# Performance work log

Hardware: AMD Instinct MI355X
Metric: run time of the kernel (lower is better)

Reference implementation:

```python
import jax, jax.numpy as jnp
import numpy as np


def _conv(x, w, pad):
    return jax.lax.conv_general_dilated(
        x, w, (1, 1), [(pad, pad), (pad, pad)],
        dimension_numbers=('NCHW', 'OIHW', 'NCHW'))


def _avgpool2(x):
    B, C, H, W = x.shape
    return x.reshape(B, C, H // 2, 2, W // 2, 2).mean(axis=(3, 5))


def setup_inputs() -> dict:
    key = jax.random.key(0)
    ks = jax.random.split(key, 10)
    B = 1024
    x = jax.random.uniform(ks[0], (B, 1, 28, 28), jnp.float32)
    # depthwise-separable conv params (in=1 -> depthwise is a plain 3x3 conv)
    dw_w = jax.random.normal(ks[1], (1, 1, 3, 3), jnp.float32) * 0.3
    pw_w = jax.random.normal(ks[2], (32, 1, 1, 1), jnp.float32) * 0.3
    pw_b = jax.random.normal(ks[3], (32,), jnp.float32) * 0.05
    # fixed 4-qubit entangling unitary (real orthogonal 16x16), stand-in for tq.RandomLayer(n_ops=8)
    U = jnp.asarray(np.linalg.qr(np.random.default_rng(0).standard_normal((16, 16)))[0],
                    jnp.float32)
    fus_w = jax.random.normal(ks[4], (128, 36, 3, 3), jnp.float32) * (1.0 / np.sqrt(36 * 9))
    fus_b = jax.random.normal(ks[5], (128,), jnp.float32) * 0.05
    F = 128 * 7 * 7
    cls_w = jax.random.normal(ks[6], (10, F), jnp.float32) * (1.0 / np.sqrt(F))
    cls_b = jax.random.normal(ks[7], (10,), jnp.float32) * 0.05
    reg_w = jax.random.normal(ks[8], (1, F), jnp.float32) * (1.0 / np.sqrt(F))
    reg_b = jax.random.normal(ks[9], (1,), jnp.float32) * 0.05
    return {'x': x, 'dw_w': dw_w, 'pw_w': pw_w, 'pw_b': pw_b, 'U': U,
            'fus_w': fus_w, 'fus_b': fus_b, 'cls_w': cls_w, 'cls_b': cls_b,
            'reg_w': reg_w, 'reg_b': reg_b}


def _quantum_patches(x, U):
    # x: (B,1,28,28) -> 14x14 grid of 2x2 patches, 4 RY angles per patch
    B = x.shape[0]
    p = x.reshape(B, 14, 2, 14, 2).transpose(0, 1, 3, 2, 4).reshape(B, 14, 14, 4)
    h = 0.5 * p
    a = jnp.stack([jnp.cos(h), jnp.sin(h)], axis=-1)       # (B,14,14,4,2)
    # RY-encoded product state |psi> = kron over 4 wires -> 16 real amplitudes
    amp = jnp.einsum('...i,...j,...k,...l->...ijkl',
                     a[..., 0, :], a[..., 1, :], a[..., 2, :], a[..., 3, :]
                     ).reshape(B, 14, 14, 16)
    state = amp @ U.T                                       # entangling layer
    probs = state * state
    idx = jnp.arange(16)
    # PauliZ expectation per wire; wire 0 is the most significant bit
    signs = 1.0 - 2.0 * (((idx[None, :] >> (3 - jnp.arange(4)[:, None])) & 1)
                         .astype(jnp.float32))              # (4,16)
    meas = probs @ signs.T                                  # (B,14,14,4)
    # replicate torch.cat(patches,dim=1).view(B,4,14,14): flat row-major then reshape
    return meas.reshape(B, 14 * 14 * 4).reshape(B, 4, 14, 14)


def reference(x, dw_w, pw_w, pw_b, U, fus_w, fus_b, cls_w, cls_b, reg_w, reg_b):
    B = x.shape[0]
    out_ds = _conv(_conv(x, dw_w, 1), pw_w, 0) + pw_b[None, :, None, None]  # (B,32,28,28)
    out_q = _quantum_patches(x, U)                                          # (B,4,14,14)
    out = jnp.concatenate([_avgpool2(out_ds), out_q], axis=1)               # (B,36,14,14)
    out = jax.nn.relu(_conv(out, fus_w, 1) + fus_b[None, :, None, None])    # (B,128,14,14)
    out = _avgpool2(out)                                                    # (B,128,7,7)
    flat = out.reshape(B, -1)
    logits = flat @ cls_w.T + cls_b
    aux = flat @ reg_w.T + reg_b
    return (logits, aux)
```

## Files before the change

### kernel.cpp

```cpp
#include <hip/hip_runtime.h>
#include <math.h>


typedef __bf16 bf16x8 __attribute__((ext_vector_type(8)));
typedef float  f32x16 __attribute__((ext_vector_type(16)));

union Pack8 { __bf16 h[8]; uint4 v; };

__global__ __launch_bounds__(256) void prep(
    const float* __restrict__ fus_w,
    const float* __restrict__ cls_w,
    const float* __restrict__ reg_w,
    __bf16* __restrict__ bfrag,
    float* __restrict__ clsTT)
{
    const int gid = blockIdx.x * 256 + threadIdx.x;
    if (gid < 55296) {
        const int j    = gid & 7;
        const int frag = gid >> 3;
        const int lane = frag & 63;
        const int rest = frag >> 6;
        const int m  = rest % 27;
        const int nt = rest / 27;
        const int t  = m / 3, ks = m - t * 3;
        const int n  = nt * 32 + (lane & 31);
        const int ic = ks * 16 + (lane >> 5) * 8 + j;
        const float v = (ic < 36) ? fus_w[n * 324 + ic * 9 + t] : 0.f;
        bfrag[gid] = (__bf16)v;
    } else if (gid < 55296 + 68992) {
        const int g2 = gid - 55296;
        const int k  = g2 / 6272;
        const int f  = g2 - k * 6272;
        const float v = (k < 10) ? cls_w[g2] : reg_w[f];
        const int oc   = f / 49;
        const int cell = f - oc * 49;
        const int nt = oc >> 5, l31 = oc & 31;
        const int mt = cell >> 3, r = cell & 7, q = r >> 1, hk = r & 1;
        clsTT[((((k * 4 + nt) * 7 + mt) * 4 + q) * 2 + hk) * 32 + l31] = v;
    } else if (gid < 55296 + 68992 + 9856) {
        const int g3  = gid - 55296 - 68992;
        const int k   = g3 / 896;
        const int rem = g3 - k * 896;
        const int oc  = rem / 7;
        const int cell = 49 + (rem - oc * 7);
        const int nt = oc >> 5, l31 = oc & 31;
        const int mt = cell >> 3, r = cell & 7, q = r >> 1, hk = r & 1;
        clsTT[((((k * 4 + nt) * 7 + mt) * 4 + q) * 2 + hk) * 32 + l31] = 0.f;
    }
}

__global__ __launch_bounds__(256, 4) void quanv_fused(
    const float* __restrict__ x,
    const float* __restrict__ dw_w,
    const float* __restrict__ pw_w,
    const float* __restrict__ pw_b,
    const float* __restrict__ U,
    const __bf16* __restrict__ bfrag,
    const float* __restrict__ fus_b,
    const float* __restrict__ clsTT,
    const float* __restrict__ cls_b,
    const float* __restrict__ reg_b,
    float* __restrict__ out,
    int B)
{
    __shared__ __align__(16) __bf16 actT[256 * 48];
    __shared__ float xs[784];
    __shared__ float red[48];

    const int b   = blockIdx.x;
    const int tid = threadIdx.x;
    const float* xb = x + b * 784;

    {
        uint4 z; z.x = 0; z.y = 0; z.z = 0; z.w = 0;
        for (int i = tid; i < 1536; i += 256) ((uint4*)actT)[i] = z;
        for (int i = tid; i < 784; i += 256) xs[i] = xb[i];
    }
    __syncthreads();

    if (tid < 196) {
        const int i = tid / 14, j = tid % 14;
        const int Y = 2 * i, X = 2 * j;

        float w9[9];
        #pragma unroll
        for (int t = 0; t < 9; ++t) w9[t] = dw_w[t];
        float dsum = 0.f;
        #pragma unroll
        for (int dy = 0; dy < 2; ++dy) {
            #pragma unroll
            for (int dx = 0; dx < 2; ++dx) {
                const int cy = Y + dy, cx = X + dx;
                #pragma unroll
                for (int ky = 0; ky < 3; ++ky) {
                    const int yy = cy + ky - 1;
                    if (yy < 0 || yy > 27) continue;
                    #pragma unroll
                    for (int kx = 0; kx < 3; ++kx) {
                        const int xx = cx + kx - 1;
                        if (xx < 0 || xx > 27) continue;
                        dsum += xs[yy * 28 + xx] * w9[ky * 3 + kx];
                    }
                }
            }
        }
        const float dpool = 0.25f * dsum;

        const int sp_o  = (i + 1) * 16 + (j + 1);
        const int rot_o = (i + 1) % 6;
        #pragma unroll
        for (int c8 = 0; c8 < 4; ++c8) {
            Pack8 pk;
            #pragma unroll
            for (int e = 0; e < 8; ++e)
                pk.h[e] = (__bf16)(pw_w[c8 * 8 + e] * dpool + pw_b[c8 * 8 + e]);
            int slot = c8 + rot_o; if (slot >= 6) slot -= 6;
            ((uint4*)actT)[sp_o * 6 + slot] = pk.v;
        }

        const float p0 = xs[Y * 28 + X],       p1 = xs[Y * 28 + X + 1];
        const float p2 = xs[(Y + 1) * 28 + X], p3 = xs[(Y + 1) * 28 + X + 1];
        float c0, s0, c1, s1, c2, s2, c3, s3;
        sincosf(0.5f * p0, &s0, &c0);
        sincosf(0.5f * p1, &s1, &c1);
        sincosf(0.5f * p2, &s2, &c2);
        sincosf(0.5f * p3, &s3, &c3);
        float a01[4] = {c0 * c1, c0 * s1, s0 * c1, s0 * s1};
        float a23[4] = {c2 * c3, c2 * s3, s2 * c3, s2 * s3};
        float amp[16];
        #pragma unroll
        for (int hi = 0; hi < 4; ++hi)
            #pragma unroll
            for (int lo = 0; lo < 4; ++lo)
                amp[hi * 4 + lo] = a01[hi] * a23[lo];

        float meas[4] = {0.f, 0.f, 0.f, 0.f};
        #pragma unroll
        for (int m = 0; m < 16; ++m) {
            float st = 0.f;
            #pragma unroll
            for (int n = 0; n < 16; ++n) st = fmaf(U[m * 16 + n], amp[n], st);
            const float pm = st * st;
            meas[0] += ((m >> 3) & 1) ? -pm : pm;
            meas[1] += ((m >> 2) & 1) ? -pm : pm;
            meas[2] += ((m >> 1) & 1) ? -pm : pm;
            meas[3] += (m & 1) ? -pm : pm;
        }
        const int fbase = i * 56 + j * 4;
        #pragma unroll
        for (int w = 0; w < 4; ++w) {
            const int f  = fbase + w;
            const int ch = f / 196;
            const int sp = f - ch * 196;
            const int r2 = sp / 14 + 1, c2i = sp % 14 + 1;
            const int sp2 = r2 * 16 + c2i;
            int slot = 4 + r2 % 6; if (slot >= 6) slot -= 6;
            actT[sp2 * 48 + slot * 8 + ch] = (__bf16)meas[w];
        }
    }
    __syncthreads();

    const int lane = tid & 63, nt = tid >> 6;
    const int l31  = lane & 31, hk = lane >> 5;
    const float fb_l = fus_b[nt * 32 + l31];

    float a11[11];
    #pragma unroll
    for (int k = 0; k < 11; ++k) a11[k] = 0.f;

    for (int mt = 0; mt < 7; ++mt) {
        const int mp   = mt * 32 + l31;
        const int cell = mp >> 2;
        const int cc = (cell < 49) ? cell : 48;
        const int py = (cc * 9363) >> 16;
        const int px = cc - py * 7;
        const int yy = 2 * py + ((mp >> 1) & 1);
        const int xx = 2 * px + (mp & 1);
        const int rowbase = yy * 16 + xx;
        const int ym6 = yy - 6 * ((yy * 43) >> 8);

        const bf16x8* bpv = (const bf16x8*)bfrag + (nt * 27 * 64 + lane);
        asm volatile("" : "+v"(bpv));

        f32x16 acc = {0.f,0.f,0.f,0.f,0.f,0.f,0.f,0.f,
                      0.f,0.f,0.f,0.f,0.f,0.f,0.f,0.f};

        #pragma unroll 1
        for (int t = 0; t < 9; ++t) {
            const int ky = (t * 11) >> 5;
            const int kx = t - 3 * ky;
            int rot = ym6 + ky; if (rot >= 6) rot -= 6;
            const int row = rowbase + ky * 16 + kx;
            #pragma unroll
            for (int ks = 0; ks < 3; ++ks) {
                int slot = 2 * ks + hk + rot; if (slot >= 6) slot -= 6;
                const bf16x8 af = *(const bf16x8*)(actT + row * 48 + slot * 8);
                const bf16x8 bf = bpv[(t * 3 + ks) * 64];
                acc = __builtin_amdgcn_mfma_f32_32x32x16_bf16(af, bf, acc, 0, 0, 0);
            }
        }

        #pragma unroll
        for (int q = 0; q < 4; ++q) {
            float pv = 0.f;
            #pragma unroll
            for (int s = 0; s < 4; ++s) {
                const float v = acc[q * 4 + s] + fb_l;
                pv += (v > 0.f ? v : 0.f);
            }
            pv *= 0.25f;
            const float* cw = clsTT + (((nt * 7 + mt) * 4 + q) * 2 + hk) * 32 + l31;
            #pragma unroll
            for (int k = 0; k < 11; ++k)
                a11[k] = fmaf(pv, cw[k * 7168], a11[k]);
        }
    }
    __syncthreads();

    const int wv = tid >> 6;
    #pragma unroll
    for (int k = 0; k < 11; ++k) {
        float a = a11[k];
        #pragma unroll
        for (int off = 32; off > 0; off >>= 1) a += __shfl_down(a, off, 64);
        if (lane == 0) red[k * 4 + wv] = a;
    }
    __syncthreads();
    if (tid < 11) {
        const float v = red[tid * 4] + red[tid * 4 + 1] + red[tid * 4 + 2] + red[tid * 4 + 3];
        if (tid < 10) out[b * 10 + tid] = v + cls_b[tid];
        else          out[B * 10 + b]   = v + reg_b[0];
    }
}

extern "C" void kernel_launch(void* const* d_in, const int* in_sizes, int n_in,
                              void* d_out, int out_size, void* d_ws, size_t ws_size,
                              hipStream_t stream) {
    const float* x    = (const float*)d_in[0];
    const float* dw_w = (const float*)d_in[1];
    const float* pw_w = (const float*)d_in[2];
    const float* pw_b = (const float*)d_in[3];
    const float* U    = (const float*)d_in[4];
    const float* fw   = (const float*)d_in[5];
    const float* fb   = (const float*)d_in[6];
    const float* cw   = (const float*)d_in[7];
    const float* cb   = (const float*)d_in[8];
    const float* rw   = (const float*)d_in[9];
    const float* rb   = (const float*)d_in[10];
    const int B = in_sizes[0] / 784;

    __bf16* bfrag = (__bf16*)d_ws;
    float*  clsTT = (float*)((char*)d_ws + 110592);

    prep<<<(55296 + 68992 + 9856 + 255) / 256, 256, 0, stream>>>(fw, cw, rw, bfrag, clsTT);
    quanv_fused<<<B, 256, 0, stream>>>(x, dw_w, pw_w, pw_b, U, bfrag, fb,
                                       clsTT, cb, rb, (float*)d_out, B);
}
```

Measured before the change: 125.7 us.

## Process two M-tiles per pass sharing B fragments with prefetch

The fusion-conv MFMA loop now handles two 32-row M tiles at once, so each loaded weight fragment from global memory feeds two MFMA chains instead of one. The next tap's three B fragments are also prefetched into registers one iteration ahead. Fewer global weight loads and more independent MFMAs in flight should hide latency better. The cost is higher register pressure from two accumulators plus the prefetch buffers under a launch bound of 4 blocks per CU.

```diff
diff --git a/kernel.cpp b/kernel.cpp
--- a/kernel.cpp
+++ b/kernel.cpp
@@ -49,6 +49,80 @@
     }
 }
 
+template<int NM>
+__device__ __forceinline__ void conv_group(
+    const int mt0, const int l31, const int hk, const int nt,
+    const __bf16* __restrict__ actT, const bf16x8* __restrict__ bpv,
+    const float fb_l, const float* __restrict__ clsTT, float* a11)
+{
+    int rowbase[NM], ym6v[NM];
+    #pragma unroll
+    for (int g = 0; g < NM; ++g) {
+        const int mp = (mt0 + g) * 32 + l31;
+        const int cell = mp >> 2;
+        const int cc = (cell < 49) ? cell : 48;
+        const int py = (cc * 9363) >> 16;
+        const int px = cc - py * 7;
+        const int yy = 2 * py + ((mp >> 1) & 1);
+        const int xx = 2 * px + (mp & 1);
+        rowbase[g] = yy * 16 + xx;
+        ym6v[g]    = yy - 6 * ((yy * 43) >> 8);
+    }
+
+    f32x16 acc[NM];
+    #pragma unroll
+    for (int g = 0; g < NM; ++g)
+        #pragma unroll
+        for (int e = 0; e < 16; ++e) acc[g][e] = 0.f;
+
+    bf16x8 nb0 = bpv[0], nb1 = bpv[64], nb2 = bpv[128];
+
+    #pragma unroll 1
+    for (int t = 0; t < 9; ++t) {
+        const bf16x8 b0 = nb0, b1 = nb1, b2 = nb2;
+        if (t < 8) {
+            nb0 = bpv[(t * 3 + 3) * 64];
+            nb1 = bpv[(t * 3 + 4) * 64];
+            nb2 = bpv[(t * 3 + 5) * 64];
+        }
+        const int ky = (t * 11) >> 5;
+        const int kx = t - 3 * ky;
+        #pragma unroll
+        for (int g = 0; g < NM; ++g) {
+            int rot = ym6v[g] + ky; if (rot >= 6) rot -= 6;
+            const int row = rowbase[g] + ky * 16 + kx;
+            int s0 = hk + rot;     if (s0 >= 6) s0 -= 6;
+            int s1 = 2 + hk + rot; if (s1 >= 6) s1 -= 6;
+            int s2 = 4 + hk + rot; if (s2 >= 6) s2 -= 6;
+            const bf16x8 af0 = *(const bf16x8*)(actT + row * 48 + s0 * 8);
+            acc[g] = __builtin_amdgcn_mfma_f32_32x32x16_bf16(af0, b0, acc[g], 0, 0, 0);
+            const bf16x8 af1 = *(const bf16x8*)(actT + row * 48 + s1 * 8);
+            acc[g] = __builtin_amdgcn_mfma_f32_32x32x16_bf16(af1, b1, acc[g], 0, 0, 0);
+            const bf16x8 af2 = *(const bf16x8*)(actT + row * 48 + s2 * 8);
+            acc[g] = __builtin_amdgcn_mfma_f32_32x32x16_bf16(af2, b2, acc[g], 0, 0, 0);
+        }
+    }
+
+    #pragma unroll
+    for (int g = 0; g < NM; ++g) {
+        const int mt = mt0 + g;
+        #pragma unroll
+        for (int q = 0; q < 4; ++q) {
+            float pv = 0.f;
+            #pragma unroll
+            for (int s = 0; s < 4; ++s) {
+                const float v = acc[g][q * 4 + s] + fb_l;
+                pv += (v > 0.f ? v : 0.f);
+            }
+            pv *= 0.25f;
+            const float* cw = clsTT + (((nt * 7 + mt) * 4 + q) * 2 + hk) * 32 + l31;
+            #pragma unroll
+            for (int k = 0; k < 11; ++k)
+                a11[k] = fmaf(pv, cw[k * 7168], a11[k]);
+        }
+    }
+}
+
 __global__ __launch_bounds__(256, 4) void quanv_fused(
     const float* __restrict__ x,
     const float* __restrict__ dw_w,
@@ -163,58 +237,16 @@
     const int lane = tid & 63, nt = tid >> 6;
     const int l31  = lane & 31, hk = lane >> 5;
     const float fb_l = fus_b[nt * 32 + l31];
+    const bf16x8* __restrict__ bpv = (const bf16x8*)bfrag + (nt * 27 * 64 + lane);
 
     float a11[11];
     #pragma unroll
     for (int k = 0; k < 11; ++k) a11[k] = 0.f;
 
-    for (int mt = 0; mt < 7; ++mt) {
-        const int mp   = mt * 32 + l31;
-        const int cell = mp >> 2;
-        const int cc = (cell < 49) ? cell : 48;
-        const int py = (cc * 9363) >> 16;
-        const int px = cc - py * 7;
-        const int yy = 2 * py + ((mp >> 1) & 1);
-        const int xx = 2 * px + (mp & 1);
-        const int rowbase = yy * 16 + xx;
-        const int ym6 = yy - 6 * ((yy * 43) >> 8);
-
-        const bf16x8* bpv = (const bf16x8*)bfrag + (nt * 27 * 64 + lane);
-        asm volatile("" : "+v"(bpv));
-
-        f32x16 acc = {0.f,0.f,0.f,0.f,0.f,0.f,0.f,0.f,
-                      0.f,0.f,0.f,0.f,0.f,0.f,0.f,0.f};
-
-        #pragma unroll 1
-        for (int t = 0; t < 9; ++t) {
-            const int ky = (t * 11) >> 5;
-            const int kx = t - 3 * ky;
-            int rot = ym6 + ky; if (rot >= 6) rot -= 6;
-            const int row = rowbase + ky * 16 + kx;
-            #pragma unroll
-            for (int ks = 0; ks < 3; ++ks) {
-                int slot = 2 * ks + hk + rot; if (slot >= 6) slot -= 6;
-                const bf16x8 af = *(const bf16x8*)(actT + row * 48 + slot * 8);
-                const bf16x8 bf = bpv[(t * 3 + ks) * 64];
-                acc = __builtin_amdgcn_mfma_f32_32x32x16_bf16(af, bf, acc, 0, 0, 0);
-            }
-        }
-
-        #pragma unroll
-        for (int q = 0; q < 4; ++q) {
-            float pv = 0.f;
-            #pragma unroll
-            for (int s = 0; s < 4; ++s) {
-                const float v = acc[q * 4 + s] + fb_l;
-                pv += (v > 0.f ? v : 0.f);
-            }
-            pv *= 0.25f;
-            const float* cw = clsTT + (((nt * 7 + mt) * 4 + q) * 2 + hk) * 32 + l31;
-            #pragma unroll
-            for (int k = 0; k < 11; ++k)
-                a11[k] = fmaf(pv, cw[k * 7168], a11[k]);
-        }
-    }
+    conv_group<2>(0, l31, hk, nt, actT, bpv, fb_l, clsTT, a11);
+    conv_group<2>(2, l31, hk, nt, actT, bpv, fb_l, clsTT, a11);
+    conv_group<2>(4, l31, hk, nt, actT, bpv, fb_l, clsTT, a11);
+    conv_group<1>(6, l31, hk, nt, actT, bpv, fb_l, clsTT, a11);
     __syncthreads();
 
     const int wv = tid >> 6;
```

New measurement: 343.7 us. 173% more time.
